# Kernel tuning notes

Measured on AMD Instinct MI355X. Metric: run time of the kernel, lower is better.

The kernel has to match this reference:

```python
import jax, jax.numpy as jnp
import numpy as np

N = 8192
IN_F = 256
OUT_F = 128
E = 262144
ALPHA = 0.2  # LeakyReLU negative slope
NEG_INF = -9e15


def setup_inputs() -> dict:
    key = jax.random.key(0)
    k_h, k_e, k_w, k_bl, k_a, k_ba = jax.random.split(key, 6)
    h = jax.random.normal(k_h, (N, IN_F), dtype=jnp.float32)
    edge_index = jax.random.randint(k_e, (2, E), 0, N, dtype=jnp.int64)
    # nn.Linear(in_features, out_features): weight [out, in], bias [out]
    lim_w = 1.0 / np.sqrt(IN_F)
    W = jax.random.uniform(k_w, (OUT_F, IN_F), minval=-lim_w, maxval=lim_w, dtype=jnp.float32)
    b_lin = jax.random.uniform(k_bl, (OUT_F,), minval=-lim_w, maxval=lim_w, dtype=jnp.float32)
    # nn.Linear(2*out_features, 1): weight [1, 2*out], bias [1]
    lim_a = 1.0 / np.sqrt(2 * OUT_F)
    a = jax.random.uniform(k_a, (1, 2 * OUT_F), minval=-lim_a, maxval=lim_a, dtype=jnp.float32)
    b_att = jax.random.uniform(k_ba, (1,), minval=-lim_a, maxval=lim_a, dtype=jnp.float32)
    return {"h": h, "edge_index": edge_index, "W": W, "b_lin": b_lin, "a": a, "b_att": b_att}


def reference(h, edge_index, W, b_lin, a, b_att):
    n = h.shape[0]
    Wh = h @ W.T + b_lin  # [N, F_out]
    # a . [Wh_i || Wh_j] + b == Wh_i.a1 + Wh_j.a2 + b  (exact decomposition of the
    # concat-pairwise attention linear; avoids materializing [N, N, 2F])
    a1 = a[0, :OUT_F]
    a2 = a[0, OUT_F:]
    s1 = Wh @ a1  # [N]
    s2 = Wh @ a2  # [N]
    e = jax.nn.leaky_relu(s1[:, None] + s2[None, :] + b_att[0], negative_slope=ALPHA)  # [N, N]
    # dense adjacency mask from edge_index (to_dense_adj semantics)
    adj = jnp.zeros((n, n), dtype=jnp.float32).at[edge_index[0], edge_index[1]].set(1.0)
    attention = jnp.where(adj > 0, e, jnp.float32(NEG_INF))
    attention = jax.nn.softmax(attention, axis=1)
    h_prime = attention @ Wh  # [N, F_out]
    return jax.nn.elu(h_prime)
```

## Files before the change

### kernel.cpp

```cpp
#include <hip/hip_runtime.h>
#include <hip/hip_bf16.h>
#include <math.h>

#define N_NODES 8192
#define IN_FEAT 256
#define OUT_FEAT 128
#define NUM_E 262144
#define LRELU_ALPHA 0.2f
#define CAP 128
#define BM_W 256

typedef __bf16 bf16x8 __attribute__((ext_vector_type(8)));
typedef float f32x4 __attribute__((ext_vector_type(4)));

__global__ __launch_bounds__(256) void k_gemm_scatter(const float* __restrict__ h,
                                                      const float* __restrict__ W,
                                                      const float* __restrict__ b_lin,
                                                      const float* __restrict__ a_att,
                                                      const float* __restrict__ b_att,
                                                      const int* __restrict__ ei,
                                                      __hip_bfloat16* __restrict__ Whb,
                                                      float* __restrict__ s1,
                                                      float* __restrict__ s2,
                                                      int* __restrict__ deg,
                                                      int* __restrict__ elist) {
    const int tid = threadIdx.x;

    const int e0 = blockIdx.x * 512 + tid * 2;
    const int2 er = *(const int2*)&ei[e0];
    const int2 ec = *(const int2*)&ei[NUM_E + e0];

    const int lane = tid & 63;
    const int w    = tid >> 6;
    const int m    = lane & 15;
    const int quad = lane >> 4;
    const int r0   = blockIdx.x * 16;
    const int wcol = w * 32;

    f32x4 acc[2] = {};

    const float* hrow = h + (r0 + m) * IN_FEAT + quad * 8;
    #pragma unroll
    for (int ks = 0; ks < 8; ++ks) {
        const int k = ks * 32;
        float4 ha = *(const float4*)(hrow + k);
        float4 hb = *(const float4*)(hrow + k + 4);
        bf16x8 af;
        af[0] = (__bf16)ha.x; af[1] = (__bf16)ha.y; af[2] = (__bf16)ha.z; af[3] = (__bf16)ha.w;
        af[4] = (__bf16)hb.x; af[5] = (__bf16)hb.y; af[6] = (__bf16)hb.z; af[7] = (__bf16)hb.w;
        #pragma unroll
        for (int nt = 0; nt < 2; ++nt) {
            const float* wp = W + (wcol + nt * 16 + m) * IN_FEAT + quad * 8 + k;
            float4 wa = *(const float4*)(wp);
            float4 wb = *(const float4*)(wp + 4);
            bf16x8 bfv;
            bfv[0] = (__bf16)wa.x; bfv[1] = (__bf16)wa.y; bfv[2] = (__bf16)wa.z; bfv[3] = (__bf16)wa.w;
            bfv[4] = (__bf16)wb.x; bfv[5] = (__bf16)wb.y; bfv[6] = (__bf16)wb.z; bfv[7] = (__bf16)wb.w;
            acc[nt] = __builtin_amdgcn_mfma_f32_16x16x32_bf16(af, bfv, acc[nt], 0, 0, 0);
        }
    }

    {
        int p;
        p = atomicAdd(&deg[er.x], 1); if (p < CAP) elist[er.x * CAP + p] = ec.x;
        p = atomicAdd(&deg[er.y], 1); if (p < CAP) elist[er.y * CAP + p] = ec.y;
    }

    float p1[4] = {0.f, 0.f, 0.f, 0.f};
    float p2[4] = {0.f, 0.f, 0.f, 0.f};
    #pragma unroll
    for (int nt = 0; nt < 2; ++nt) {
        const int col = wcol + nt * 16 + m;
        const float bl = b_lin[col];
        const float a1 = a_att[col];
        const float a2 = a_att[OUT_FEAT + col];
        #pragma unroll
        for (int reg = 0; reg < 4; ++reg) {
            const float v = acc[nt][reg] + bl;
            const int row = r0 + quad * 4 + reg;
            Whb[row * OUT_FEAT + col] = __float2bfloat16(v);
            p1[reg] = fmaf(v, a1, p1[reg]);
            p2[reg] = fmaf(v, a2, p2[reg]);
        }
    }
    #pragma unroll
    for (int off = 1; off < 16; off <<= 1) {
        #pragma unroll
        for (int reg = 0; reg < 4; ++reg) {
            p1[reg] += __shfl_xor(p1[reg], off, 64);
            p2[reg] += __shfl_xor(p2[reg], off, 64);
        }
    }
    __shared__ float red1[16][4];
    __shared__ float red2[16][4];
    if (m == 0) {
        #pragma unroll
        for (int reg = 0; reg < 4; ++reg) {
            red1[quad * 4 + reg][w] = p1[reg];
            red2[quad * 4 + reg][w] = p2[reg];
        }
    }
    __syncthreads();
    if (tid < 16) {
        s1[r0 + tid] = red1[tid][0] + red1[tid][1] + red1[tid][2] + red1[tid][3] + b_att[0];
    } else if (tid >= 64 && tid < 80) {
        const int r = tid - 64;
        s2[r0 + r] = red2[r][0] + red2[r][1] + red2[r][2] + red2[r][3];
    }
}

__global__ __launch_bounds__(128) void k_aggr(const int* __restrict__ deg,
                                              const int* __restrict__ elist,
                                              const float* __restrict__ s1,
                                              const float* __restrict__ s2,
                                              const __hip_bfloat16* __restrict__ Whb,
                                              float* __restrict__ out) {
    __shared__ unsigned int bm[BM_W];
    __shared__ float el[CAP];
    __shared__ int   jl[CAP];
    __shared__ float colred[4][128];
    __shared__ float dred[4];
    const int tid = threadIdx.x;
    const int w = tid >> 6, lane = tid & 63;
    const int i = blockIdx.x;

    const int jraw = elist[i * CAP + tid];
    const int nr   = deg[i];
    const float s1i = s1[i];
    const float s2p = s2[jraw & (N_NODES - 1)];
    bm[tid] = 0u; bm[tid + 128] = 0u;
    __syncthreads();
    const int n = nr < CAP ? nr : CAP;

    if (tid < n) {
        float wt = 0.f;
        jl[tid] = jraw;
        const unsigned int bit = 1u << (jraw & 31);
        const unsigned int old = atomicOr(&bm[jraw >> 5], bit);
        if (!(old & bit)) {
            float v = s1i + s2p;
            v = v > 0.f ? v : LRELU_ALPHA * v;
            wt = __expf(v);
        }
        el[tid] = wt;
    }
    __syncthreads();

    const int half = lane >> 5;
    const int slot = w * 2 + half;
    const int cb = (lane & 31) * 4;
    float a0 = 0.f, a1 = 0.f, a2 = 0.f, a3 = 0.f, ds = 0.f;
    int t = slot;
    if (t < n) {
        float wv = el[t];
        int j = jl[t];
        uint2 u = *(const uint2*)&Whb[j * OUT_FEAT + cb];
        for (t += 4; t < n; t += 4) {
            const float wvn = el[t];
            const int jn = jl[t];
            const uint2 un = *(const uint2*)&Whb[jn * OUT_FEAT + cb];
            union { unsigned int ui; float f; } c0, c1, c2, c3;
            c0.ui = u.x << 16; c1.ui = u.x & 0xffff0000u;
            c2.ui = u.y << 16; c3.ui = u.y & 0xffff0000u;
            a0 = fmaf(wv, c0.f, a0);
            a1 = fmaf(wv, c1.f, a1);
            a2 = fmaf(wv, c2.f, a2);
            a3 = fmaf(wv, c3.f, a3);
            ds += wv;
            wv = wvn; u = un;
        }
        union { unsigned int ui; float f; } c0, c1, c2, c3;
        c0.ui = u.x << 16; c1.ui = u.x & 0xffff0000u;
        c2.ui = u.y << 16; c3.ui = u.y & 0xffff0000u;
        a0 = fmaf(wv, c0.f, a0);
        a1 = fmaf(wv, c1.f, a1);
        a2 = fmaf(wv, c2.f, a2);
        a3 = fmaf(wv, c3.f, a3);
        ds += wv;
    }
    colred[slot][cb]     = a0;
    colred[slot][cb + 1] = a1;
    colred[slot][cb + 2] = a2;
    colred[slot][cb + 3] = a3;
    if ((lane & 31) == 0) dred[slot] = ds;
    __syncthreads();

    float o;
    if (n > 0) {
        const float denom = dred[0] + dred[1] + dred[2] + dred[3];
        o = (colred[0][tid] + colred[1][tid] + colred[2][tid] + colred[3][tid]) / denom;
    } else {
        float acc = 0.f;
        for (int r = 0; r < N_NODES; ++r) acc += __bfloat162float(Whb[r * OUT_FEAT + tid]);
        o = acc * (1.f / (float)N_NODES);
    }
    out[i * OUT_FEAT + tid] = o > 0.f ? o : expm1f(o);
}

extern "C" void kernel_launch(void* const* d_in, const int* in_sizes, int n_in,
                              void* d_out, int out_size, void* d_ws, size_t ws_size,
                              hipStream_t stream) {
    const float* h     = (const float*)d_in[0];
    const int*   ei    = (const int*)d_in[1];
    const float* W     = (const float*)d_in[2];
    const float* b_lin = (const float*)d_in[3];
    const float* a     = (const float*)d_in[4];
    const float* b_att = (const float*)d_in[5];
    float* out = (float*)d_out;

    char* ws = (char*)d_ws;
    __hip_bfloat16* Whb = (__hip_bfloat16*)(ws);
    float* s1    = (float*)(ws + 2097152);
    float* s2    = (float*)(ws + 2097152 + 32768);
    int*   elist = (int*)(ws + 2097152 + 65536);
    int*   deg   = (int*)(ws + 2097152 + 65536 + 4194304);

    hipMemsetAsync(deg, 0, N_NODES * sizeof(int), stream);
    k_gemm_scatter<<<N_NODES / 16, 256, 0, stream>>>(h, W, b_lin, a, b_att, ei,
                                                     Whb, s1, s2, deg, elist);
    k_aggr<<<N_NODES, 128, 0, stream>>>(deg, elist, s1, s2, Whb, out);
}
```

Baseline: 101.2 us.

## Pre-convert inputs to bf16 in prep kernel and widen aggregation blocks

Adds a prep kernel that converts h and W to bf16 once and zeroes the degree array, replacing the memset launch. The GEMM kernel then loads bf16 fragments directly instead of converting fp32 per block. The aggregation kernel moves to 256 threads with 8 slots and an 8-deep batched gather loop to raise memory-level parallelism. The cost is an extra full pass over h (read fp32, write bf16) plus one more kernel launch.

```diff
diff --git a/kernel.cpp b/kernel.cpp
--- a/kernel.cpp
+++ b/kernel.cpp
@@ -11,10 +11,30 @@
 #define BM_W 256
 
 typedef __bf16 bf16x8 __attribute__((ext_vector_type(8)));
+typedef __bf16 bf16x4 __attribute__((ext_vector_type(4)));
 typedef float f32x4 __attribute__((ext_vector_type(4)));
 
-__global__ __launch_bounds__(256) void k_gemm_scatter(const float* __restrict__ h,
-                                                      const float* __restrict__ W,
+__global__ __launch_bounds__(256) void k_prep(const float* __restrict__ h,
+                                              const float* __restrict__ W,
+                                              __bf16* __restrict__ hb,
+                                              __bf16* __restrict__ Wb,
+                                              int* __restrict__ deg) {
+    const int g = blockIdx.x * 256 + threadIdx.x;
+    const float4 f = *(const float4*)&h[g * 4];
+    bf16x4 o;
+    o[0] = (__bf16)f.x; o[1] = (__bf16)f.y; o[2] = (__bf16)f.z; o[3] = (__bf16)f.w;
+    *(bf16x4*)&hb[g * 4] = o;
+    if (g < N_NODES) {
+        deg[g] = 0;
+        const float4 wf = *(const float4*)&W[g * 4];
+        bf16x4 wo;
+        wo[0] = (__bf16)wf.x; wo[1] = (__bf16)wf.y; wo[2] = (__bf16)wf.z; wo[3] = (__bf16)wf.w;
+        *(bf16x4*)&Wb[g * 4] = wo;
+    }
+}
+
+__global__ __launch_bounds__(256) void k_gemm_scatter(const __bf16* __restrict__ hb,
+                                                      const __bf16* __restrict__ Wb,
                                                       const float* __restrict__ b_lin,
                                                       const float* __restrict__ a_att,
                                                       const float* __restrict__ b_att,
@@ -39,23 +59,15 @@
 
     f32x4 acc[2] = {};
 
-    const float* hrow = h + (r0 + m) * IN_FEAT + quad * 8;
+    const __bf16* hrow = hb + (r0 + m) * IN_FEAT + quad * 8;
+    const __bf16* wrow0 = Wb + (wcol + m) * IN_FEAT + quad * 8;
     #pragma unroll
     for (int ks = 0; ks < 8; ++ks) {
         const int k = ks * 32;
-        float4 ha = *(const float4*)(hrow + k);
-        float4 hb = *(const float4*)(hrow + k + 4);
-        bf16x8 af;
-        af[0] = (__bf16)ha.x; af[1] = (__bf16)ha.y; af[2] = (__bf16)ha.z; af[3] = (__bf16)ha.w;
-        af[4] = (__bf16)hb.x; af[5] = (__bf16)hb.y; af[6] = (__bf16)hb.z; af[7] = (__bf16)hb.w;
+        const bf16x8 af = *(const bf16x8*)(hrow + k);
         #pragma unroll
         for (int nt = 0; nt < 2; ++nt) {
-            const float* wp = W + (wcol + nt * 16 + m) * IN_FEAT + quad * 8 + k;
-            float4 wa = *(const float4*)(wp);
-            float4 wb = *(const float4*)(wp + 4);
-            bf16x8 bfv;
-            bfv[0] = (__bf16)wa.x; bfv[1] = (__bf16)wa.y; bfv[2] = (__bf16)wa.z; bfv[3] = (__bf16)wa.w;
-            bfv[4] = (__bf16)wb.x; bfv[5] = (__bf16)wb.y; bfv[6] = (__bf16)wb.z; bfv[7] = (__bf16)wb.w;
+            const bf16x8 bfv = *(const bf16x8*)(wrow0 + nt * 16 * IN_FEAT + k);
             acc[nt] = __builtin_amdgcn_mfma_f32_16x16x32_bf16(af, bfv, acc[nt], 0, 0, 0);
         }
     }
@@ -109,7 +121,7 @@
     }
 }
 
-__global__ __launch_bounds__(128) void k_aggr(const int* __restrict__ deg,
+__global__ __launch_bounds__(256) void k_aggr(const int* __restrict__ deg,
                                               const int* __restrict__ elist,
                                               const float* __restrict__ s1,
                                               const float* __restrict__ s2,
@@ -118,17 +130,17 @@
     __shared__ unsigned int bm[BM_W];
     __shared__ float el[CAP];
     __shared__ int   jl[CAP];
-    __shared__ float colred[4][128];
-    __shared__ float dred[4];
+    __shared__ float colred[8][128];
+    __shared__ float dred[8];
     const int tid = threadIdx.x;
     const int w = tid >> 6, lane = tid & 63;
     const int i = blockIdx.x;
 
-    const int jraw = elist[i * CAP + tid];
+    const int jraw = (tid < CAP) ? elist[i * CAP + tid] : 0;
     const int nr   = deg[i];
     const float s1i = s1[i];
     const float s2p = s2[jraw & (N_NODES - 1)];
-    bm[tid] = 0u; bm[tid + 128] = 0u;
+    bm[tid] = 0u;
     __syncthreads();
     const int n = nr < CAP ? nr : CAP;
 
@@ -150,33 +162,30 @@
     const int slot = w * 2 + half;
     const int cb = (lane & 31) * 4;
     float a0 = 0.f, a1 = 0.f, a2 = 0.f, a3 = 0.f, ds = 0.f;
-    int t = slot;
-    if (t < n) {
-        float wv = el[t];
-        int j = jl[t];
-        uint2 u = *(const uint2*)&Whb[j * OUT_FEAT + cb];
-        for (t += 4; t < n; t += 4) {
-            const float wvn = el[t];
-            const int jn = jl[t];
-            const uint2 un = *(const uint2*)&Whb[jn * OUT_FEAT + cb];
-            union { unsigned int ui; float f; } c0, c1, c2, c3;
-            c0.ui = u.x << 16; c1.ui = u.x & 0xffff0000u;
-            c2.ui = u.y << 16; c3.ui = u.y & 0xffff0000u;
-            a0 = fmaf(wv, c0.f, a0);
-            a1 = fmaf(wv, c1.f, a1);
-            a2 = fmaf(wv, c2.f, a2);
-            a3 = fmaf(wv, c3.f, a3);
-            ds += wv;
-            wv = wvn; u = un;
-        }
-        union { unsigned int ui; float f; } c0, c1, c2, c3;
-        c0.ui = u.x << 16; c1.ui = u.x & 0xffff0000u;
-        c2.ui = u.y << 16; c3.ui = u.y & 0xffff0000u;
-        a0 = fmaf(wv, c0.f, a0);
-        a1 = fmaf(wv, c1.f, a1);
-        a2 = fmaf(wv, c2.f, a2);
-        a3 = fmaf(wv, c3.f, a3);
-        ds += wv;
+    for (int base = slot; base < n; base += 64) {
+        uint2 u[8]; float wv[8];
+        #pragma unroll
+        for (int q = 0; q < 8; ++q) {
+            const int t = base + q * 8;
+            if (t < n) {
+                wv[q] = el[t];
+                u[q] = *(const uint2*)&Whb[jl[t] * OUT_FEAT + cb];
+            }
+        }
+        #pragma unroll
+        for (int q = 0; q < 8; ++q) {
+            const int t = base + q * 8;
+            if (t < n) {
+                union { unsigned int ui; float f; } c0, c1, c2, c3;
+                c0.ui = u[q].x << 16; c1.ui = u[q].x & 0xffff0000u;
+                c2.ui = u[q].y << 16; c3.ui = u[q].y & 0xffff0000u;
+                a0 = fmaf(wv[q], c0.f, a0);
+                a1 = fmaf(wv[q], c1.f, a1);
+                a2 = fmaf(wv[q], c2.f, a2);
+                a3 = fmaf(wv[q], c3.f, a3);
+                ds += wv[q];
+            }
+        }
     }
     colred[slot][cb]     = a0;
     colred[slot][cb + 1] = a1;
@@ -185,16 +194,20 @@
     if ((lane & 31) == 0) dred[slot] = ds;
     __syncthreads();
 
-    float o;
-    if (n > 0) {
-        const float denom = dred[0] + dred[1] + dred[2] + dred[3];
-        o = (colred[0][tid] + colred[1][tid] + colred[2][tid] + colred[3][tid]) / denom;
-    } else {
-        float acc = 0.f;
-        for (int r = 0; r < N_NODES; ++r) acc += __bfloat162float(Whb[r * OUT_FEAT + tid]);
-        o = acc * (1.f / (float)N_NODES);
-    }
-    out[i * OUT_FEAT + tid] = o > 0.f ? o : expm1f(o);
+    if (tid < OUT_FEAT) {
+        float o;
+        if (n > 0) {
+            const float denom = dred[0] + dred[1] + dred[2] + dred[3]
+                              + dred[4] + dred[5] + dred[6] + dred[7];
+            o = (colred[0][tid] + colred[1][tid] + colred[2][tid] + colred[3][tid]
+               + colred[4][tid] + colred[5][tid] + colred[6][tid] + colred[7][tid]) / denom;
+        } else {
+            float acc = 0.f;
+            for (int r = 0; r < N_NODES; ++r) acc += __bfloat162float(Whb[r * OUT_FEAT + tid]);
+            o = acc * (1.f / (float)N_NODES);
+        }
+        out[i * OUT_FEAT + tid] = o > 0.f ? o : expm1f(o);
+    }
 }
 
 extern "C" void kernel_launch(void* const* d_in, const int* in_sizes, int n_in,
@@ -211,12 +224,14 @@
     char* ws = (char*)d_ws;
     __hip_bfloat16* Whb = (__hip_bfloat16*)(ws);
     float* s1    = (float*)(ws + 2097152);
-    float* s2    = (float*)(ws + 2097152 + 32768);
-    int*   elist = (int*)(ws + 2097152 + 65536);
-    int*   deg   = (int*)(ws + 2097152 + 65536 + 4194304);
-
-    hipMemsetAsync(deg, 0, N_NODES * sizeof(int), stream);
-    k_gemm_scatter<<<N_NODES / 16, 256, 0, stream>>>(h, W, b_lin, a, b_att, ei,
+    float* s2    = (float*)(ws + 2129920);
+    int*   elist = (int*)(ws + 2162688);
+    int*   deg   = (int*)(ws + 6356992);
+    __bf16* hb   = (__bf16*)(ws + 6389760);
+    __bf16* Wb   = (__bf16*)(ws + 10584064);
+
+    k_prep<<<524288 / 256, 256, 0, stream>>>(h, W, hb, Wb, deg);
+    k_gemm_scatter<<<N_NODES / 16, 256, 0, stream>>>(hb, Wb, b_lin, a, b_att, ei,
                                                      Whb, s1, s2, deg, elist);
-    k_aggr<<<N_NODES, 128, 0, stream>>>(deg, elist, s1, s2, Whb, out);
-}
+    k_aggr<<<N_NODES, 256, 0, stream>>>(deg, elist, s1, s2, Whb, out);
+}
```

Measured after the change: 98.12 us. 1.03x faster.
